# Performance work log

Hardware: AMD Instinct MI355X
Metric: run time of the kernel (lower is better)

## Reference

```python
import jax, jax.numpy as jnp
import numpy as np

K_DIM = 1024
N_HEADS = 16
HEAD = K_DIM // N_HEADS


def setup_inputs() -> dict:
    key = jax.random.key(0)
    kx, kq, kk, kv, ko = jax.random.split(key, 5)
    b, t = 2, 2048
    scale = 1.0 / np.sqrt(K_DIM)
    x = jax.random.normal(kx, (b, t, K_DIM), dtype=jnp.float32)
    # nn.Linear(k, k, bias=False): y = x @ W.T, W has shape [k, k]
    Wq = jax.random.normal(kq, (K_DIM, K_DIM), dtype=jnp.float32) * scale
    Wk = jax.random.normal(kk, (K_DIM, K_DIM), dtype=jnp.float32) * scale
    Wv = jax.random.normal(kv, (K_DIM, K_DIM), dtype=jnp.float32) * scale
    Wo = jax.random.normal(ko, (K_DIM, K_DIM), dtype=jnp.float32) * scale
    return {"x": x, "Wq": Wq, "Wk": Wk, "Wv": Wv, "Wo": Wo}


def reference(x, Wq, Wk, Wv, Wo):
    b, t, k = x.shape
    h, hs = N_HEADS, HEAD
    # projections (torch Linear: x @ W.T), split heads -> [b, h, t, hs]
    Q = (x @ Wq.T).reshape(b, t, h, hs).transpose(0, 2, 1, 3)
    Kt = (x @ Wk.T).reshape(b, t, h, hs).transpose(0, 2, 1, 3)
    V = (x @ Wv.T).reshape(b, t, h, hs).transpose(0, 2, 1, 3)
    # NOTE: original scales by sqrt(k) (model dim), not sqrt(head_size)
    scores = jnp.einsum('bhqd,bhkd->bhqk', Q, Kt) / jnp.sqrt(jnp.asarray(k, x.dtype))
    W = jax.nn.softmax(scores, axis=-1)
    O = jnp.einsum('bhqk,bhkd->bhqd', W, V)  # [b, h, t, hs]
    O = O.transpose(0, 2, 1, 3).reshape(b, t, k)
    return O @ Wo.T
```

## Files before the change

kernel.cpp:

```cpp
#include <hip/hip_runtime.h>
#include <hip/hip_bf16.h>

#define N_HEADS 16
#define HEAD 64
#define B_SZ 2
#define T_SZ 2048
#define KD 1024
#define M_TOT (B_SZ * T_SZ)

typedef short bf16x8 __attribute__((ext_vector_type(8)));
typedef short bf16x4 __attribute__((ext_vector_type(4)));
typedef float f32x4  __attribute__((ext_vector_type(4)));

#define MFMA32(a, b, c) __builtin_amdgcn_mfma_f32_16x16x32_bf16((a), (b), (c), 0, 0, 0)

__device__ __forceinline__ ushort f2bf(float f) {
    __hip_bfloat16 h = __float2bfloat16(f);
    return *reinterpret_cast<ushort*>(&h);
}

__device__ __forceinline__ ushort f2bf_fast(float f) {
    return (ushort)((__float_as_uint(f) + 0x8000u) >> 16);
}

__device__ __forceinline__ float exp2fast(float x) {
#if __has_builtin(__builtin_amdgcn_exp2f)
    return __builtin_amdgcn_exp2f(x);
#else
    return exp2f(x);
#endif
}

__device__ __forceinline__ void gl2lds16(const ushort* g, void* l) {
    __builtin_amdgcn_global_load_lds(
        (const __attribute__((address_space(1))) unsigned int*)g,
        (__attribute__((address_space(3))) unsigned int*)l, 16, 0, 0);
}

#define RAW_BARRIER() do { asm volatile("" ::: "memory"); \
                           __builtin_amdgcn_s_barrier();  \
                           asm volatile("" ::: "memory"); } while (0)

__global__ void cvt_all(const float* __restrict__ x,
                        const float* __restrict__ Wq, const float* __restrict__ Wk,
                        const float* __restrict__ Wv, const float* __restrict__ Wo,
                        ushort* __restrict__ xb, ushort* __restrict__ wb) {
    const int NX = (M_TOT * KD) / 4;
    const int NW = (KD * KD) / 4;
    int i = blockIdx.x * blockDim.x + threadIdx.x;
    float4 v;
    ushort* dst;
    if (i < NX) {
        v = reinterpret_cast<const float4*>(x)[i];
        dst = xb + (size_t)i * 4;
    } else {
        int j = i - NX;
        int w = j >> 18;
        int r = j & (NW - 1);
        const float* s = (w == 0) ? Wq : (w == 1) ? Wk : (w == 2) ? Wv : Wo;
        v = reinterpret_cast<const float4*>(s)[r];
        dst = wb + (size_t)w * KD * KD + (size_t)r * 4;
    }
    ushort4 o;
    o.x = f2bf(v.x); o.y = f2bf(v.y); o.z = f2bf(v.z); o.w = f2bf(v.w);
    *reinterpret_cast<ushort4*>(dst) = o;
}

__global__ __launch_bounds__(512) void gemm_qkv(const ushort* __restrict__ A,
                                                const ushort* __restrict__ Bm,
                                                ushort* __restrict__ Qbase) {
    const int bm = blockIdx.x;
    const int bn = blockIdx.y;
    __shared__ alignas(128) char As[16384];
    __shared__ alignas(128) char Bs[16384];
    const int tid = threadIdx.x;
    const int lane = tid & 63;
    const int w = tid >> 6;
    const int wr = w >> 2, wc = w & 3;
    const int r15 = lane & 15, q4 = lane >> 4;
    const int sl8 = lane >> 3;
    const int scol = (((lane & 7) * 16) ^ (sl8 << 4)) >> 1;

    f32x4 acc[4][2] = {};

    for (int k0 = 0; k0 < 1024; k0 += 64) {
        #pragma unroll
        for (int rr = 0; rr < 2; ++rr) {
            int r = rr * 64 + w * 8 + sl8;
            gl2lds16(A  + (size_t)(bm * 128 + r) * 1024 + k0 + scol, &As[(rr * 64 + w * 8) * 128]);
            gl2lds16(Bm + (size_t)(bn * 128 + r) * 1024 + k0 + scol, &Bs[(rr * 64 + w * 8) * 128]);
        }
        asm volatile("s_waitcnt vmcnt(0)" ::: "memory");
        RAW_BARRIER();

        #pragma unroll
        for (int kk = 0; kk < 2; ++kk) {
            bf16x8 af[4], bfr[2];
            #pragma unroll
            for (int m = 0; m < 4; ++m) {
                int row = wr * 64 + m * 16 + r15;
                af[m] = *(const bf16x8*)(&As[row * 128 + ((kk * 64 + q4 * 16) ^ ((row & 7) << 4))]);
            }
            #pragma unroll
            for (int n = 0; n < 2; ++n) {
                int row = wc * 32 + n * 16 + r15;
                bfr[n] = *(const bf16x8*)(&Bs[row * 128 + ((kk * 64 + q4 * 16) ^ ((row & 7) << 4))]);
            }
            #pragma unroll
            for (int m = 0; m < 4; ++m)
                #pragma unroll
                for (int n = 0; n < 2; ++n)
                    acc[m][n] = MFMA32(af[m], bfr[n], acc[m][n]);
        }
        RAW_BARRIER();
    }

    const size_t seg = (size_t)32 * 2048 * 64;
    const int which = bn >> 3;
    const int row0 = bm * 128 + wr * 64;
    const int col0w = bn * 128 + wc * 32;
    char* ep = ((w & 4) ? Bs : As) + (w & 3) * 4096;

    if (which == 2) {
        #pragma unroll
        for (int m = 0; m < 4; ++m)
            #pragma unroll
            for (int n = 0; n < 2; ++n)
                #pragma unroll
                for (int i = 0; i < 4; ++i) {
                    int dl = n * 16 + r15;
                    int trow = m * 16 + q4 * 4 + i;
                    int blk = (trow >> 2) & 7;
                    int npos = (blk < 4) ? (blk << 1) : ((blk << 1) - 7);
                    int tcol = (trow & 32) | (npos << 2) | (trow & 3);
                    *(ushort*)(ep + dl * 128 + ((tcol * 2) ^ ((dl & 7) << 4))) =
                        f2bf(acc[m][n][i]);
                }
        const int head = (col0w & 1023) >> 6;
        const int d0 = col0w & 63;
        const int bidx = row0 >> 11;
        const int t0 = row0 & 2047;
        #pragma unroll
        for (int j = 0; j < 4; ++j) {
            int d = (lane >> 3) + j * 8;
            int c = lane & 7;
            bf16x8 vv = *(const bf16x8*)(ep + d * 128 + ((c * 16) ^ ((d & 7) << 4)));
            *(bf16x8*)(&Qbase[2 * seg + ((size_t)(bidx * 16 + head) * 64 + d0 + d) * 2048 +
                              t0 + c * 8]) = vv;
        }
    } else {
        const float sc = (which == 0) ? 0.045084439f : 1.0f;
        #pragma unroll
        for (int m = 0; m < 4; ++m)
            #pragma unroll
            for (int n = 0; n < 2; ++n)
                #pragma unroll
                for (int i = 0; i < 4; ++i) {
                    int row = m * 16 + q4 * 4 + i;
                    int colb = (n * 16 + r15) * 2;
                    *(ushort*)(ep + row * 64 + (colb ^ ((row & 3) << 4))) =
                        f2bf(acc[m][n][i] * sc);
                }
        const int head = (col0w & 1023) >> 6;
        const int dhalf = col0w & 63;
        #pragma unroll
        for (int j = 0; j < 8; ++j) {
            int row = (lane >> 3) + j * 8;
            bf16x4 vv = *(const bf16x4*)(ep + row * 64 +
                                         (((lane & 7) * 8) ^ ((row & 3) << 4)));
            int grow = row0 + row;
            int bidx = grow >> 11;
            int t = grow & 2047;
            *(bf16x4*)(&Qbase[(size_t)which * seg +
                              (((size_t)(bidx * 16 + head) * 2048 + t) * 64) + dhalf +
                              (lane & 7) * 4]) = vv;
        }
    }
}

__global__ __launch_bounds__(512) void gemm_o(const ushort* __restrict__ A,
                                              const ushort* __restrict__ Bm,
                                              float* __restrict__ C) {
    const int bm = blockIdx.x;
    const int bn = blockIdx.y;
    __shared__ alignas(128) char As[16384];
    __shared__ alignas(128) char Bs[8192];
    const int tid = threadIdx.x;
    const int lane = tid & 63;
    const int w = tid >> 6;
    const int wr = w >> 2, wc = w & 3;
    const int r15 = lane & 15, q4 = lane >> 4;
    const int sl8 = lane >> 3;
    const int scol = (((lane & 7) * 16) ^ (sl8 << 4)) >> 1;

    f32x4 acc[4] = {};

    for (int k0 = 0; k0 < 1024; k0 += 64) {
        #pragma unroll
        for (int rr = 0; rr < 2; ++rr) {
            int r = rr * 64 + w * 8 + sl8;
            gl2lds16(A + (size_t)(bm * 128 + r) * 1024 + k0 + scol, &As[(rr * 64 + w * 8) * 128]);
        }
        {
            int r = w * 8 + sl8;
            gl2lds16(Bm + (size_t)(bn * 64 + r) * 1024 + k0 + scol, &Bs[(w * 8) * 128]);
        }
        asm volatile("s_waitcnt vmcnt(0)" ::: "memory");
        RAW_BARRIER();

        #pragma unroll
        for (int kk = 0; kk < 2; ++kk) {
            bf16x8 af[4], bfr;
            #pragma unroll
            for (int m = 0; m < 4; ++m) {
                int row = wr * 64 + m * 16 + r15;
                af[m] = *(const bf16x8*)(&As[row * 128 + ((kk * 64 + q4 * 16) ^ ((row & 7) << 4))]);
            }
            {
                int row = wc * 16 + r15;
                bfr = *(const bf16x8*)(&Bs[row * 128 + ((kk * 64 + q4 * 16) ^ ((row & 7) << 4))]);
            }
            #pragma unroll
            for (int m = 0; m < 4; ++m)
                acc[m] = MFMA32(af[m], bfr, acc[m]);
        }
        RAW_BARRIER();
    }

    const int row0 = bm * 128 + wr * 64;
    const int col0 = bn * 64 + wc * 16;
    #pragma unroll
    for (int m = 0; m < 4; ++m)
        #pragma unroll
        for (int i = 0; i < 4; ++i)
            C[(size_t)(row0 + m * 16 + q4 * 4 + i) * 1024 + col0 + r15] = acc[m][i];
}

__global__ __launch_bounds__(1024) void attn_fwd(const ushort* __restrict__ Qh,
                                                 const ushort* __restrict__ Kh,
                                                 const ushort* __restrict__ Vt,
                                                 ushort* __restrict__ Ob) {
    const int bh = blockIdx.x;
    const int qt = blockIdx.y;
    const int tid = threadIdx.x;
    const int lane = tid & 63, w = tid >> 6;
    const int grp = w >> 3, wl = w & 7;
    const int r15 = lane & 15, q4 = lane >> 4;

    const ushort* Qp = Qh + (size_t)bh * T_SZ * HEAD;
    const ushort* Kp = Kh + (size_t)bh * T_SZ * HEAD;
    const ushort* Vp = Vt + (size_t)bh * HEAD * T_SZ;

    __shared__ alignas(16) char SMEM[65536];
    char* Kbuf = SMEM + grp * 32768;
    char* Vbuf = Kbuf + 16384;

    const int srow = wl * 8 + (lane >> 3);
    const int sslot = (lane & 7) * 16;
    const int ssb = (sslot ^ ((srow & 7) << 4)) >> 1;
    const int kvbase = grp << 10;

    const int q0 = qt * 256 + wl * 32;
    bf16x8 qf[2][2];
    #pragma unroll
    for (int cc = 0; cc < 2; ++cc) {
        qf[cc][0] = *(const bf16x8*)(&Qp[(size_t)(q0 + cc * 16 + r15) * 64 + q4 * 8]);
        qf[cc][1] = *(const bf16x8*)(&Qp[(size_t)(q0 + cc * 16 + r15) * 64 + 32 + q4 * 8]);
    }

    const bf16x8 ones8 = {0x3F80, 0x3F80, 0x3F80, 0x3F80, 0x3F80, 0x3F80, 0x3F80, 0x3F80};

    f32x4 acc[2][4] = {};
    f32x4 acc_l[2] = {};

    #define STAGE(buf, kv0)                                                      \
        {                                                                        \
            gl2lds16(Kp + (size_t)(kvbase + (kv0) + srow) * 64 + ssb,            \
                     Kbuf + (buf) * 8192 + wl * 8 * 128);                        \
            gl2lds16(Vp + (size_t)srow * 2048 + kvbase + (kv0) + ssb,            \
                     Vbuf + (buf) * 8192 + wl * 8 * 128);                        \
        }

    STAGE(0, 0);
    int cur = 0;
    for (int it = 0; it < 16; ++it) {
        STAGE(cur ^ 1, ((it + 1) & 15) * 64);
        asm volatile("s_waitcnt vmcnt(2)" ::: "memory");
        RAW_BARRIER();

        const char* Ks = Kbuf + cur * 8192;
        const char* Vs = Vbuf + cur * 8192;

        bf16x8 kf[4][2];
        #pragma unroll
        for (int t4 = 0; t4 < 4; ++t4) {
            int row = t4 * 16 + r15;
            int sw = (row & 7) << 4;
            kf[t4][0] = *(const bf16x8*)(&Ks[row * 128 + ((q4 * 16) ^ sw)]);
            kf[t4][1] = *(const bf16x8*)(&Ks[row * 128 + ((64 + q4 * 16) ^ sw)]);
        }
        bf16x8 vf8[2][4];
        #pragma unroll
        for (int dt = 0; dt < 4; ++dt) {
            int row = dt * 16 + r15;
            int sw = (row & 7) << 4;
            #pragma unroll
            for (int t32 = 0; t32 < 2; ++t32)
                vf8[t32][dt] = *(const bf16x8*)(&Vs[row * 128 + ((t32 * 64 + q4 * 16) ^ sw)]);
        }

        f32x4 z[2][4];
        #pragma unroll
        for (int cc = 0; cc < 2; ++cc)
            #pragma unroll
            for (int t4 = 0; t4 < 4; ++t4) {
                f32x4 zz = {};
                zz = MFMA32(kf[t4][0], qf[cc][0], zz);
                zz = MFMA32(kf[t4][1], qf[cc][1], zz);
                z[cc][t4] = zz;
            }

        bf16x8 pb8[2][2];
        #pragma unroll
        for (int cc = 0; cc < 2; ++cc)
            #pragma unroll
            for (int t32 = 0; t32 < 2; ++t32)
                #pragma unroll
                for (int i = 0; i < 4; ++i) {
                    pb8[cc][t32][i]     = (short)f2bf_fast(exp2fast(z[cc][2 * t32][i]));
                    pb8[cc][t32][4 + i] = (short)f2bf_fast(exp2fast(z[cc][2 * t32 + 1][i]));
                }

        #pragma unroll
        for (int t32 = 0; t32 < 2; ++t32) {
            #pragma unroll
            for (int dt = 0; dt < 4; ++dt)
                #pragma unroll
                for (int cc = 0; cc < 2; ++cc)
                    acc[cc][dt] = MFMA32(vf8[t32][dt], pb8[cc][t32], acc[cc][dt]);
            #pragma unroll
            for (int cc = 0; cc < 2; ++cc)
                acc_l[cc] = MFMA32(ones8, pb8[cc][t32], acc_l[cc]);
        }

        RAW_BARRIER();
        cur ^= 1;
    }
    #undef STAGE

    asm volatile("s_waitcnt vmcnt(0)" ::: "memory");
    __syncthreads();

    float l0 = acc_l[0][0], l1 = acc_l[1][0];
    {
        float* MB = (float*)SMEM;
        #pragma unroll
        for (int rnd = 0; rnd < 2; ++rnd) {
            __syncthreads();
            if (grp == 1 && (wl >> 2) == rnd) {
                float* p = MB + (((wl & 3) * 64 + lane) * 34);
                #pragma unroll
                for (int cc = 0; cc < 2; ++cc)
                    #pragma unroll
                    for (int dt = 0; dt < 4; ++dt) {
                        *(float2*)(p + (cc * 4 + dt) * 4)     = make_float2(acc[cc][dt][0], acc[cc][dt][1]);
                        *(float2*)(p + (cc * 4 + dt) * 4 + 2) = make_float2(acc[cc][dt][2], acc[cc][dt][3]);
                    }
                *(float2*)(p + 32) = make_float2(l0, l1);
            }
            __syncthreads();
            if (grp == 0 && (wl >> 2) == rnd) {
                const float* p = MB + (((wl & 3) * 64 + lane) * 34);
                #pragma unroll
                for (int cc = 0; cc < 2; ++cc)
                    #pragma unroll
                    for (int dt = 0; dt < 4; ++dt)
                        #pragma unroll
                        for (int i = 0; i < 4; ++i)
                            acc[cc][dt][i] += p[(cc * 4 + dt) * 4 + i];
                l0 += p[32];
                l1 += p[33];
            }
        }
    }

    if (grp == 0) {
        const int b = bh >> 4, h = bh & 15;
        #pragma unroll
        for (int cc = 0; cc < 2; ++cc) {
            float inv = 1.0f / (cc ? l1 : l0);
            int q = q0 + cc * 16 + r15;
            #pragma unroll
            for (int dt = 0; dt < 4; ++dt) {
                ushort4 o;
                o.x = f2bf(acc[cc][dt][0] * inv);
                o.y = f2bf(acc[cc][dt][1] * inv);
                o.z = f2bf(acc[cc][dt][2] * inv);
                o.w = f2bf(acc[cc][dt][3] * inv);
                *(ushort4*)(&Ob[((size_t)(b * T_SZ + q)) * KD + h * HEAD + dt * 16 + q4 * 4]) = o;
            }
        }
    }
}

extern "C" void kernel_launch(void* const* d_in, const int* in_sizes, int n_in,
                              void* d_out, int out_size, void* d_ws, size_t ws_size,
                              hipStream_t stream) {
    const float* x  = (const float*)d_in[0];
    const float* Wq = (const float*)d_in[1];
    const float* Wk = (const float*)d_in[2];
    const float* Wv = (const float*)d_in[3];
    const float* Wo = (const float*)d_in[4];

    char* ws = (char*)d_ws;
    const size_t MB = 1024 * 1024;
    ushort* xb    = (ushort*)(ws + 0);
    ushort* Wqkvb = (ushort*)(ws + 8  * MB);
    ushort* Wob   = Wqkvb + 3 * (size_t)KD * KD;
    ushort* Qh    = (ushort*)(ws + 16 * MB);
    ushort* Kh    = (ushort*)(ws + 24 * MB);
    ushort* VhT   = (ushort*)(ws + 32 * MB);
    ushort* Ob    = (ushort*)(ws + 40 * MB);

    {
        int total4 = (M_TOT * KD) / 4 + KD * KD;
        cvt_all<<<total4 / 256, 256, 0, stream>>>(x, Wq, Wk, Wv, Wo, xb, Wqkvb);
    }

    gemm_qkv<<<dim3(32, 24), 512, 0, stream>>>(xb, Wqkvb, Qh);
    attn_fwd<<<dim3(32, 8), 1024, 0, stream>>>(Qh, Kh, VhT, Ob);
    gemm_o<<<dim3(32, 16), 512, 0, stream>>>(Ob, Wob, (float*)d_out);
}
```

Before: 99.52 us.

## Enlarge QKV GEMM tiles to 256x256 with double-buffered LDS and interleaved MFMA

The QKV projection GEMM now uses 256x256 block tiles with 128KB of LDS, double-buffered so global-to-LDS loads for the next k-step overlap MFMA work on the current one. MFMA issue is split into quadrants with priority raised around them. The epilogue is reworked so each wave writes a full head (64 columns) with wider 16-byte stores. The grid shrinks to 192 blocks, which may underfill the 256 CUs, and the large LDS footprint limits occupancy to one block per CU.

```diff
diff --git a/kernel.cpp b/kernel.cpp
--- a/kernel.cpp
+++ b/kernel.cpp
@@ -71,8 +71,7 @@
                                                 ushort* __restrict__ Qbase) {
     const int bm = blockIdx.x;
     const int bn = blockIdx.y;
-    __shared__ alignas(128) char As[16384];
-    __shared__ alignas(128) char Bs[16384];
+    __shared__ alignas(128) char SM[131072];
     const int tid = threadIdx.x;
     const int lane = tid & 63;
     const int w = tid >> 6;
@@ -81,101 +80,146 @@
     const int sl8 = lane >> 3;
     const int scol = (((lane & 7) * 16) ^ (sl8 << 4)) >> 1;
 
-    f32x4 acc[4][2] = {};
-
-    for (int k0 = 0; k0 < 1024; k0 += 64) {
-        #pragma unroll
-        for (int rr = 0; rr < 2; ++rr) {
-            int r = rr * 64 + w * 8 + sl8;
-            gl2lds16(A  + (size_t)(bm * 128 + r) * 1024 + k0 + scol, &As[(rr * 64 + w * 8) * 128]);
-            gl2lds16(Bm + (size_t)(bn * 128 + r) * 1024 + k0 + scol, &Bs[(rr * 64 + w * 8) * 128]);
-        }
+    f32x4 acc[8][4] = {};
+
+#define QSTAGE_A(s, kofs, h)                                                     \
+    { _Pragma("unroll")                                                          \
+      for (int inst = 0; inst < 2; ++inst) {                                     \
+          int lr = (h) * 128 + w * 16 + inst * 8;                                \
+          gl2lds16(A + (size_t)(bm * 256 + lr + sl8) * 1024 + (kofs) + scol,     \
+                   SM + (s) * 32768 + (size_t)lr * 128);                         \
+      } }
+#define QSTAGE_B(s, kofs, h)                                                     \
+    { _Pragma("unroll")                                                          \
+      for (int inst = 0; inst < 2; ++inst) {                                     \
+          int lr = (h) * 128 + w * 16 + inst * 8;                                \
+          gl2lds16(Bm + (size_t)(bn * 256 + lr + sl8) * 1024 + (kofs) + scol,    \
+                   SM + 65536 + (s) * 32768 + (size_t)lr * 128);                 \
+      } }
+#define QLOAD_A(kt, qm)                                                          \
+    { const char* Ab_ = SM + (kt) * 32768;                                       \
+      _Pragma("unroll") for (int m = 0; m < 4; ++m)                              \
+      _Pragma("unroll") for (int kk = 0; kk < 2; ++kk) {                         \
+          int row = wr * 128 + (qm) * 64 + m * 16 + r15;                         \
+          af[m * 2 + kk] = *(const bf16x8*)(&Ab_[row * 128 +                     \
+              ((kk * 64 + q4 * 16) ^ ((row & 7) << 4))]);                        \
+      } }
+#define QLOAD_B(kt, qn, dstv)                                                    \
+    { const char* Bb_ = SM + 65536 + (kt) * 32768;                               \
+      _Pragma("unroll") for (int n = 0; n < 2; ++n)                              \
+      _Pragma("unroll") for (int kk = 0; kk < 2; ++kk) {                         \
+          int row = wc * 64 + (qn) * 32 + n * 16 + r15;                          \
+          dstv[n * 2 + kk] = *(const bf16x8*)(&Bb_[row * 128 +                   \
+              ((kk * 64 + q4 * 16) ^ ((row & 7) << 4))]);                        \
+      } }
+#define QMFMA(qm, qn, bv)                                                        \
+    { __builtin_amdgcn_s_setprio(1);                                             \
+      _Pragma("unroll") for (int m = 0; m < 4; ++m)                              \
+      _Pragma("unroll") for (int n = 0; n < 2; ++n)                              \
+      _Pragma("unroll") for (int kk = 0; kk < 2; ++kk)                           \
+          acc[(qm) * 4 + m][(qn) * 2 + n] =                                      \
+              MFMA32(af[m * 2 + kk], bv[n * 2 + kk],                             \
+                     acc[(qm) * 4 + m][(qn) * 2 + n]);                           \
+      __builtin_amdgcn_s_setprio(0); }
+
+    QSTAGE_A(0, 0, 0); QSTAGE_A(0, 0, 1); QSTAGE_B(0, 0, 0); QSTAGE_B(0, 0, 1);
+    asm volatile("s_waitcnt vmcnt(0)" ::: "memory");
+    RAW_BARRIER();
+
+    bf16x8 af[8], bf0[4], bf1[4];
+
+    for (int i = 0; i < 8; ++i) {
+        const int k1 = (2 * i + 1) * 64;
+        const int k2 = ((2 * i + 2) & 15) * 64;
+        QSTAGE_A(1, k1, 0); QSTAGE_A(1, k1, 1);
+        QLOAD_A(0, 0); QLOAD_B(0, 0, bf0);
+        QMFMA(0, 0, bf0);
+        RAW_BARRIER();
+        QSTAGE_B(1, k1, 0); QSTAGE_B(1, k1, 1);
+        QLOAD_B(0, 1, bf1);
+        QMFMA(0, 1, bf1);
+        RAW_BARRIER();
+        QLOAD_A(0, 1);
+        QMFMA(1, 0, bf0);
+        RAW_BARRIER();
+        QMFMA(1, 1, bf1);
         asm volatile("s_waitcnt vmcnt(0)" ::: "memory");
         RAW_BARRIER();
-
-        #pragma unroll
-        for (int kk = 0; kk < 2; ++kk) {
-            bf16x8 af[4], bfr[2];
-            #pragma unroll
-            for (int m = 0; m < 4; ++m) {
-                int row = wr * 64 + m * 16 + r15;
-                af[m] = *(const bf16x8*)(&As[row * 128 + ((kk * 64 + q4 * 16) ^ ((row & 7) << 4))]);
-            }
-            #pragma unroll
-            for (int n = 0; n < 2; ++n) {
-                int row = wc * 32 + n * 16 + r15;
-                bfr[n] = *(const bf16x8*)(&Bs[row * 128 + ((kk * 64 + q4 * 16) ^ ((row & 7) << 4))]);
-            }
-            #pragma unroll
-            for (int m = 0; m < 4; ++m)
-                #pragma unroll
-                for (int n = 0; n < 2; ++n)
-                    acc[m][n] = MFMA32(af[m], bfr[n], acc[m][n]);
-        }
+        QSTAGE_A(0, k2, 0); QSTAGE_A(0, k2, 1);
+        QLOAD_A(1, 0); QLOAD_B(1, 0, bf0);
+        QMFMA(0, 0, bf0);
+        RAW_BARRIER();
+        QSTAGE_B(0, k2, 0); QSTAGE_B(0, k2, 1);
+        QLOAD_B(1, 1, bf1);
+        QMFMA(0, 1, bf1);
+        RAW_BARRIER();
+        QLOAD_A(1, 1);
+        QMFMA(1, 0, bf0);
+        RAW_BARRIER();
+        QMFMA(1, 1, bf1);
+        asm volatile("s_waitcnt vmcnt(0)" ::: "memory");
         RAW_BARRIER();
     }
 
     const size_t seg = (size_t)32 * 2048 * 64;
-    const int which = bn >> 3;
-    const int row0 = bm * 128 + wr * 64;
-    const int col0w = bn * 128 + wc * 32;
-    char* ep = ((w & 4) ? Bs : As) + (w & 3) * 4096;
+    const int which = bn >> 2;
+    const int head = (bn & 3) * 4 + wc;
+    const int row0 = bm * 256 + wr * 128;
+    const int bidx = row0 >> 11;
+    const int t0 = row0 & 2047;
+    char* ep = SM + w * 16384;
 
     if (which == 2) {
         #pragma unroll
-        for (int m = 0; m < 4; ++m)
-            #pragma unroll
-            for (int n = 0; n < 2; ++n)
-                #pragma unroll
-                for (int i = 0; i < 4; ++i) {
-                    int dl = n * 16 + r15;
-                    int trow = m * 16 + q4 * 4 + i;
-                    int blk = (trow >> 2) & 7;
+        for (int m = 0; m < 8; ++m)
+            #pragma unroll
+            for (int nn = 0; nn < 4; ++nn)
+                #pragma unroll
+                for (int i2 = 0; i2 < 4; ++i2) {
+                    int d = nn * 16 + r15;
+                    int traw = m * 16 + q4 * 4 + i2;
+                    int blk = (traw >> 2) & 7;
                     int npos = (blk < 4) ? (blk << 1) : ((blk << 1) - 7);
-                    int tcol = (trow & 32) | (npos << 2) | (trow & 3);
-                    *(ushort*)(ep + dl * 128 + ((tcol * 2) ^ ((dl & 7) << 4))) =
-                        f2bf(acc[m][n][i]);
+                    int tp = (traw & ~31) | (npos << 2) | (traw & 3);
+                    *(ushort*)(ep + d * 256 + ((tp * 2) ^ ((d & 15) << 4))) =
+                        f2bf(acc[m][nn][i2]);
                 }
-        const int head = (col0w & 1023) >> 6;
-        const int d0 = col0w & 63;
-        const int bidx = row0 >> 11;
-        const int t0 = row0 & 2047;
-        #pragma unroll
-        for (int j = 0; j < 4; ++j) {
-            int d = (lane >> 3) + j * 8;
-            int c = lane & 7;
-            bf16x8 vv = *(const bf16x8*)(ep + d * 128 + ((c * 16) ^ ((d & 7) << 4)));
-            *(bf16x8*)(&Qbase[2 * seg + ((size_t)(bidx * 16 + head) * 64 + d0 + d) * 2048 +
+        #pragma unroll
+        for (int j = 0; j < 16; ++j) {
+            int d = (lane >> 4) + j * 4;
+            int c = lane & 15;
+            bf16x8 vv = *(const bf16x8*)(ep + d * 256 + ((c * 16) ^ ((d & 15) << 4)));
+            *(bf16x8*)(&Qbase[2 * seg + ((size_t)(bidx * 16 + head) * 64 + d) * 2048 +
                               t0 + c * 8]) = vv;
         }
     } else {
         const float sc = (which == 0) ? 0.045084439f : 1.0f;
         #pragma unroll
-        for (int m = 0; m < 4; ++m)
-            #pragma unroll
-            for (int n = 0; n < 2; ++n)
-                #pragma unroll
-                for (int i = 0; i < 4; ++i) {
-                    int row = m * 16 + q4 * 4 + i;
-                    int colb = (n * 16 + r15) * 2;
-                    *(ushort*)(ep + row * 64 + (colb ^ ((row & 3) << 4))) =
-                        f2bf(acc[m][n][i] * sc);
+        for (int m = 0; m < 8; ++m)
+            #pragma unroll
+            for (int nn = 0; nn < 4; ++nn)
+                #pragma unroll
+                for (int i2 = 0; i2 < 4; ++i2) {
+                    int t = m * 16 + q4 * 4 + i2;
+                    int dby = (nn * 16 + r15) * 2;
+                    *(ushort*)(ep + t * 128 + (dby ^ ((t & 7) << 4))) =
+                        f2bf(acc[m][nn][i2] * sc);
                 }
-        const int head = (col0w & 1023) >> 6;
-        const int dhalf = col0w & 63;
-        #pragma unroll
-        for (int j = 0; j < 8; ++j) {
+        #pragma unroll
+        for (int j = 0; j < 16; ++j) {
             int row = (lane >> 3) + j * 8;
-            bf16x4 vv = *(const bf16x4*)(ep + row * 64 +
-                                         (((lane & 7) * 8) ^ ((row & 3) << 4)));
-            int grow = row0 + row;
-            int bidx = grow >> 11;
-            int t = grow & 2047;
-            *(bf16x4*)(&Qbase[(size_t)which * seg +
-                              (((size_t)(bidx * 16 + head) * 2048 + t) * 64) + dhalf +
-                              (lane & 7) * 4]) = vv;
-        }
-    }
+            bf16x8 vv = *(const bf16x8*)(ep + row * 128 +
+                                         (((lane & 7) * 16) ^ ((row & 7) << 4)));
+            *(bf16x8*)(&Qbase[(size_t)which * seg +
+                              (((size_t)(bidx * 16 + head) * 2048 + t0 + row) * 64) +
+                              (lane & 7) * 8]) = vv;
+        }
+    }
+#undef QSTAGE_A
+#undef QSTAGE_B
+#undef QLOAD_A
+#undef QLOAD_B
+#undef QMFMA
 }
 
 __global__ __launch_bounds__(512) void gemm_o(const ushort* __restrict__ A,
@@ -427,7 +471,7 @@
         cvt_all<<<total4 / 256, 256, 0, stream>>>(x, Wq, Wk, Wv, Wo, xb, Wqkvb);
     }
 
-    gemm_qkv<<<dim3(32, 24), 512, 0, stream>>>(xb, Wqkvb, Qh);
+    gemm_qkv<<<dim3(16, 12), 512, 0, stream>>>(xb, Wqkvb, Qh);
     attn_fwd<<<dim3(32, 8), 1024, 0, stream>>>(Qh, Kh, VhT, Ob);
     gemm_o<<<dim3(32, 16), 512, 0, stream>>>(Ob, Wob, (float*)d_out);
 }
```

After: 95.92 us, median of 2. -3.6%, faster.
